# Kernel tuning notes

Measured on AMD Instinct MI355X. Metric: run time of the kernel, lower is better.

The kernel has to match this reference:

```python
import jax, jax.numpy as jnp
import numpy as np

N_E = 1024
E_DIM = 256
BETA = 0.25
PERSISTENCE = 0.1
B, T = 16, 1024


def setup_inputs() -> dict:
    key = jax.random.key(0)
    k1, k2 = jax.random.split(key)
    z = jax.random.normal(k1, (B, T, E_DIM), dtype=jnp.float32)
    # nn.Embedding(1+n_e, e_dim) init uniform(-1/n_e, 1/n_e)
    emb_weight = jax.random.uniform(k2, (N_E + 1, E_DIM), dtype=jnp.float32,
                                    minval=-1.0 / N_E, maxval=1.0 / N_E)
    return {"z": z, "emb_weight": emb_weight}


def _loss_contrast(z, ind, book):
    # z: (B,T,e), ind: (B,T) int, book: (n_e+1, e)
    z_q = book[ind]                                   # (B,T,e)
    loss_indices = jnp.sum((z - z_q) ** 2, axis=-1)   # (B,T)
    # ||z - book||^2 expanded to avoid the (B,T,n_e+1,e) intermediate
    z_sq = jnp.sum(z * z, axis=-1)                    # (B,T)
    b_sq = jnp.sum(book * book, axis=-1)              # (n_e+1,)
    cross = jnp.einsum('bte,ne->btn', z, book)        # (B,T,n_e+1)
    loss_all = z_sq[..., None] + b_sq[None, None, :] - 2.0 * cross
    lc = jnp.maximum(loss_indices[..., None] - loss_all + 1e-6 / N_E, 0.0)
    return jnp.mean(lc)


def _forward(z, emb_weight):
    zf = z.reshape(-1, E_DIM)
    d = (jnp.sum(zf * zf, axis=1, keepdims=True)
         + jnp.sum(emb_weight * emb_weight, axis=1)
         - 2.0 * (zf @ emb_weight.T)).reshape(B, T, N_E + 1)

    ind0 = jnp.clip(jnp.argmin(d[:, 0, :], axis=1), 0, N_E - 1)  # (B,)

    def step(carry, d_t):
        ind, coe = carry                              # (B,) int, (B,) f32
        d_here = jnp.take_along_axis(d_t, ind[:, None], axis=1)[:, 0]
        ind_next = jnp.minimum(ind + 1, N_E - 1)
        d_next = jnp.take_along_axis(d_t, ind_next[:, None], axis=1)[:, 0]
        stay = d_here <= d_next - coe
        ind_new = jnp.where(stay, ind, ind_next)
        coe_new = jnp.where(stay, coe + PERSISTENCE / N_E, 0.0)
        return (ind_new, coe_new), ind_new

    coe0 = jnp.zeros((B,), jnp.float32)
    _, inds = jax.lax.scan(step, (ind0, coe0), jnp.swapaxes(d[:, 1:, :], 0, 1))
    encoding_indices = jnp.concatenate([ind0[None, :], inds], axis=0).T  # (B,T)

    book_sg = jax.lax.stop_gradient(emb_weight)  # torch uses .data/.detach() everywhere
    z_q_raw = book_sg[encoding_indices]
    z_q = z + jax.lax.stop_gradient(z_q_raw - z)  # straight-through

    # non-legacy: beta * L(z, sg(book)) + L(sg(z), sg(book))
    loss = (BETA * _loss_contrast(z, encoding_indices, book_sg)
            + _loss_contrast(jax.lax.stop_gradient(z), encoding_indices, book_sg))

    v = jnp.max(encoding_indices) - jnp.min(encoding_indices)
    return z_q, loss, encoding_indices, v


def reference(z, emb_weight):
    return _forward(z, emb_weight)
```

## Files before the change

### kernel.cpp

```cpp
#include <hip/hip_runtime.h>

#define N_E   1024
#define EDIM  256
#define BB    16
#define TT    1024
#define NROW  (BB*TT)
#define NCOL  1025
#define NPAD  1152
#define PERS  (0.1f/1024.0f)
#define EPSC  (1e-6f/1024.0f)

#define OUT_LOSS 4194304
#define OUT_IDX  4194305
#define OUT_V    4210689

#define WS_ZB   0ull
#define WS_BBF  8388608ull
#define WS_BSQ  8978432ull
#define WS_E    8983552ull
#define WS_IND  84481024ull
#define WS_PART 84546560ull

typedef __attribute__((ext_vector_type(8))) short short8;
typedef __attribute__((ext_vector_type(4))) float floatx4;

__device__ __forceinline__ unsigned short f2bf(float f) {
    unsigned int u = __float_as_uint(f);
    u = (u + 0x7fffu + ((u >> 16) & 1u)) >> 16;
    return (unsigned short)u;
}

__device__ __forceinline__ float gload_f32(const float* p) {
    float r;
    asm volatile("global_load_dword %0, %1, off" : "=v"(r) : "v"(p));
    return r;
}

__global__ __launch_bounds__(256) void k0_prep(const float* __restrict__ z,
                                               const float* __restrict__ book,
                                               unsigned short* __restrict__ zb,
                                               unsigned short* __restrict__ bb,
                                               float* __restrict__ bsq) {
    int bx = blockIdx.x, tid = threadIdx.x;
    if (bx < 4096) {
        float4 v = ((const float4*)z)[bx * 256 + tid];
        size_t o = ((size_t)bx * 256 + tid) * 4;
        zb[o + 0] = f2bf(v.x); zb[o + 1] = f2bf(v.y);
        zb[o + 2] = f2bf(v.z); zb[o + 3] = f2bf(v.w);
    } else {
        int row = bx - 4096;
        float v = (row < NCOL) ? book[(size_t)row * EDIM + tid] : 0.0f;
        bb[(size_t)row * EDIM + tid] = f2bf(v);
        __shared__ float sd[256];
        sd[tid] = v * v;
        __syncthreads();
        for (int s = 128; s > 0; s >>= 1) { if (tid < s) sd[tid] += sd[tid + s]; __syncthreads(); }
        if (tid == 0) bsq[row] = sd[0];
    }
}

__global__ __launch_bounds__(256) void k1_gemm(const unsigned short* __restrict__ zb,
                                               const unsigned short* __restrict__ bb,
                                               const float* __restrict__ bsq,
                                               float* __restrict__ e) {
    int tid = threadIdx.x;
    int lane = tid & 63, w = tid >> 6;
    int mBase = blockIdx.x * 128 + (w >> 1) * 64;
    int nBase = blockIdx.y * 128 + (w & 1) * 64;
    int r = lane & 15, q = lane >> 4;

    floatx4 acc[4][4];
    #pragma unroll
    for (int i = 0; i < 4; i++)
        #pragma unroll
        for (int j = 0; j < 4; j++) acc[i][j] = (floatx4){0.f, 0.f, 0.f, 0.f};

    const short8* A = (const short8*)zb;
    const short8* Bm = (const short8*)bb;

    #pragma unroll
    for (int ks = 0; ks < 8; ks++) {
        int k8 = ks * 4 + q;
        short8 a[4], b[4];
        #pragma unroll
        for (int i = 0; i < 4; i++) a[i] = A[(size_t)(mBase + i * 16 + r) * 32 + k8];
        #pragma unroll
        for (int j = 0; j < 4; j++) b[j] = Bm[(size_t)(nBase + j * 16 + r) * 32 + k8];
        #pragma unroll
        for (int i = 0; i < 4; i++)
            #pragma unroll
            for (int j = 0; j < 4; j++)
                acc[i][j] = __builtin_amdgcn_mfma_f32_16x16x32_bf16(a[i], b[j], acc[i][j], 0, 0, 0);
    }

    float bsql[4];
    #pragma unroll
    for (int j = 0; j < 4; j++) bsql[j] = bsq[nBase + j * 16 + r];

    #pragma unroll
    for (int i = 0; i < 4; i++)
        #pragma unroll
        for (int rr = 0; rr < 4; rr++) {
            int m = mBase + i * 16 + q * 4 + rr;
            float* erow = e + (size_t)m * NPAD;
            #pragma unroll
            for (int j = 0; j < 4; j++)
                erow[nBase + j * 16 + r] = fmaf(-2.0f, acc[i][j][rr], bsql[j]);
        }
}


#define R15(X) X(0) X(1) X(2) X(3) X(4) X(5) X(6) X(7) X(8) X(9) X(10) X(11) X(12) X(13) X(14)

#define DECLA(i) float A0_##i, A1_##i, A2_##i; int q_##i;

#define LDR(S,i) { int _t = _tb + i; _t = _t < 1024 ? _t : 1023; \
                   A##S##_##i = gload_f32(_pe + (size_t)_t * NPAD); }
#define LD0(i) LDR(0,i)
#define LD1(i) LDR(1,i)
#define LD2(i) LDR(2,i)

#define QC(S,i) { float _bv = __shfl_down(A##S##_##i, 1, 64); \
                  int _qv = (int)((_bv - A##S##_##i) * QS); \
                  q_##i = _capn ? 0 : _qv; }
#define QC0(i) QC(0,i)
#define QC1(i) QC(1,i)
#define QC2(i) QC(2,i)

#define CH(i) { int _rel = ind - cb0; \
                int _qv = __builtin_amdgcn_readlane(q_##i, _rel); \
                bool _stay = (kk <= _qv); \
                int _ip1 = ind + 1; _ip1 = _ip1 < 1023 ? _ip1 : 1023; \
                ind = _stay ? ind : _ip1; \
                kk  = _stay ? kk + 1 : 0; \
                packed = (lane == i) ? ind : packed; }

#define ITER(SI, SC) { \
    int cbI = ind < 960 ? ind : 960; \
    { const float* _pe = eb + cbI + lane; int _tb = t + 45; R15(LD##SI) } \
    __builtin_amdgcn_sched_barrier(0); \
    int packed = 0; \
    R15(CH) \
    if (lane < 15 && t + lane < 1024) wind[ibase + t + lane] = packed; \
    __builtin_amdgcn_sched_barrier(0); \
    asm volatile("s_waitcnt vmcnt(31)" ::: "memory"); \
    __builtin_amdgcn_sched_barrier(0); \
    { bool _capn = (cb1 + lane == 1023); R15(QC##SC) } \
    cb0 = cb1; cb1 = cb2; cb2 = cbI; \
    t += 15; }

__global__ __launch_bounds__(256, 1) void k2_scan(const float* __restrict__ z,
                                                  const float* __restrict__ book,
                                                  const float* __restrict__ bsq,
                                                  const float* __restrict__ e,
                                                  int* __restrict__ wind) {
    __shared__ float sb[4]; __shared__ int si[4];

    int b = blockIdx.x, tid = threadIdx.x;
    int lane = tid & 63, w = tid >> 6;

    const float4* zr = (const float4*)(z + (size_t)b * TT * EDIM);
    float4 zv = zr[lane];
    float s = zv.x * zv.x + zv.y * zv.y + zv.z * zv.z + zv.w * zv.w;
    #pragma unroll
    for (int off = 32; off; off >>= 1) s += __shfl_xor(s, off, 64);
    float zsq = s;

    float best = 3.4e38f; int bidx = 0;
    for (int wi = w; wi < 17; wi += 4) {
        int n = wi * 64 + lane;
        if (n < NCOL) {
            const float4* br = (const float4*)(book + (size_t)n * EDIM);
            float c0 = 0.f, c1 = 0.f, c2 = 0.f, c3 = 0.f;
            #pragma unroll 8
            for (int k = 0; k < 64; k++) {
                float4 bo = br[k]; float4 za = zr[k];
                c0 = fmaf(za.x, bo.x, c0); c1 = fmaf(za.y, bo.y, c1);
                c2 = fmaf(za.z, bo.z, c2); c3 = fmaf(za.w, bo.w, c3);
            }
            float cr = (c0 + c1) + (c2 + c3);
            float d0 = (zsq + bsq[n]) - 2.0f * cr;
            if (d0 < best || (d0 == best && n < bidx)) { best = d0; bidx = n; }
        }
    }
    #pragma unroll
    for (int off = 32; off; off >>= 1) {
        float ob = __shfl_xor(best, off, 64);
        int   oi = __shfl_xor(bidx, off, 64);
        if (ob < best || (ob == best && oi < bidx)) { best = ob; bidx = oi; }
    }
    if (lane == 0) { sb[w] = best; si[w] = bidx; }
    __syncthreads();
    if (w != 0) return;

    best = sb[0]; bidx = si[0];
    for (int i = 1; i < 4; i++) {
        float vv = sb[i]; int ii = si[i];
        if (vv < best || (vv == best && ii < bidx)) { best = vv; bidx = ii; }
    }

    int ind = min(bidx, N_E - 1);
    int kk = 0;
    size_t ibase = (size_t)b * TT;
    if (lane == 0) wind[ibase] = ind;

    const float* eb = e + (size_t)b * TT * NPAD;
    const float QS = 1.0f / PERS;

    R15(DECLA)

    int cb0 = ind < 960 ? ind : 960;
    int cb1 = cb0, cb2 = cb0;
    { const float* _pe = eb + cb0 + lane; int _tb = 1;  R15(LD0) }
    { const float* _pe = eb + cb1 + lane; int _tb = 16; R15(LD1) }
    { const float* _pe = eb + cb2 + lane; int _tb = 31; R15(LD2) }
    asm volatile("s_waitcnt vmcnt(30)" ::: "memory");
    __builtin_amdgcn_sched_barrier(0);
    { bool _capn = (cb0 + lane == 1023); R15(QC0) }

    int t = 1;
    #pragma unroll 1
    for (int cc = 0; cc < 23; cc++) {
        ITER(0, 1)
        ITER(1, 2)
        ITER(2, 0)
    }
}

__global__ __launch_bounds__(256) void k3_loss_zq(const float* __restrict__ e,
                                                  const int* __restrict__ wind,
                                                  const float* __restrict__ book,
                                                  float* __restrict__ part,
                                                  float* __restrict__ out) {
    int rIdx = blockIdx.x, tid = threadIdx.x;
    int ind = wind[rIdx];
    const float* er = e + (size_t)rIdx * NPAD;
    float eind = er[ind];
    float p = 0.0f;
    for (int n = tid; n < NCOL; n += 256) {
        float v = eind - er[n] + EPSC;
        p += v > 0.0f ? v : 0.0f;
    }
    __shared__ float sd[256];
    sd[tid] = p; __syncthreads();
    for (int s = 128; s > 0; s >>= 1) { if (tid < s) sd[tid] += sd[tid + s]; __syncthreads(); }
    if (tid == 0) { part[rIdx] = sd[0]; out[OUT_IDX + rIdx] = (float)ind; }
    out[(size_t)rIdx * 256 + tid] = book[(size_t)ind * EDIM + tid];
}

__global__ __launch_bounds__(256) void k4_final(const float* __restrict__ part,
                                                const int* __restrict__ wind,
                                                float* __restrict__ out) {
    int tid = threadIdx.x;
    float s = 0.0f;
    for (int i = tid; i < NROW; i += 256) s += part[i];
    __shared__ float sd[256];
    sd[tid] = s; __syncthreads();
    for (int st = 128; st > 0; st >>= 1) { if (tid < st) sd[tid] += sd[tid + st]; __syncthreads(); }
    if (tid == 0) {
        int mn = wind[0], mx = wind[TT - 1];
        for (int b = 1; b < BB; b++) {
            mn = min(mn, wind[(size_t)b * TT]);
            mx = max(mx, wind[(size_t)b * TT + TT - 1]);
        }
        out[OUT_LOSS] = 1.25f * sd[0] / ((float)NROW * (float)NCOL);
        out[OUT_V] = (float)(mx - mn);
    }
}

extern "C" void kernel_launch(void* const* d_in, const int* in_sizes, int n_in,
                              void* d_out, int out_size, void* d_ws, size_t ws_size,
                              hipStream_t stream) {
    const float* z    = (const float*)d_in[0];
    const float* book = (const float*)d_in[1];
    char* ws = (char*)d_ws;
    unsigned short* zb = (unsigned short*)(ws + WS_ZB);
    unsigned short* bb = (unsigned short*)(ws + WS_BBF);
    float* bsq  = (float*)(ws + WS_BSQ);
    float* e    = (float*)(ws + WS_E);
    int*   wind = (int*)(ws + WS_IND);
    float* part = (float*)(ws + WS_PART);
    float* out  = (float*)d_out;

    hipLaunchKernelGGL(k0_prep,    dim3(4096 + 1152), dim3(256), 0, stream, z, book, zb, bb, bsq);
    hipLaunchKernelGGL(k1_gemm,    dim3(128, 9),      dim3(256), 0, stream, zb, bb, bsq, e);
    hipLaunchKernelGGL(k2_scan,    dim3(16),          dim3(256), 0, stream, z, book, bsq, e, wind);
    hipLaunchKernelGGL(k3_loss_zq, dim3(16384),       dim3(256), 0, stream, e, wind, book, part, out);
    hipLaunchKernelGGL(k4_final,   dim3(1),           dim3(256), 0, stream, part, wind, out);
}
```

Baseline: 251.4 us.

## Split scan window across half-waves and use double-buffered 10-step prefetch

```diff
diff --git a/kernel.cpp b/kernel.cpp
--- a/kernel.cpp
+++ b/kernel.cpp
@@ -110,44 +110,41 @@
 }
 
 
-#define R15(X) X(0) X(1) X(2) X(3) X(4) X(5) X(6) X(7) X(8) X(9) X(10) X(11) X(12) X(13) X(14)
-
-#define DECLA(i) float A0_##i, A1_##i, A2_##i; int q_##i;
-
-#define LDR(S,i) { int _t = _tb + i; _t = _t < 1024 ? _t : 1023; \
-                   A##S##_##i = gload_f32(_pe + (size_t)_t * NPAD); }
-#define LD0(i) LDR(0,i)
-#define LD1(i) LDR(1,i)
-#define LD2(i) LDR(2,i)
-
-#define QC(S,i) { float _bv = __shfl_down(A##S##_##i, 1, 64); \
-                  int _qv = (int)((_bv - A##S##_##i) * QS); \
-                  q_##i = _capn ? 0 : _qv; }
-#define QC0(i) QC(0,i)
-#define QC1(i) QC(1,i)
-#define QC2(i) QC(2,i)
-
-#define CH(i) { int _rel = ind - cb0; \
-                int _qv = __builtin_amdgcn_readlane(q_##i, _rel); \
-                bool _stay = (kk <= _qv); \
-                int _ip1 = ind + 1; _ip1 = _ip1 < 1023 ? _ip1 : 1023; \
-                ind = _stay ? ind : _ip1; \
-                kk  = _stay ? kk + 1 : 0; \
-                packed = (lane == i) ? ind : packed; }
-
-#define ITER(SI, SC) { \
-    int cbI = ind < 960 ? ind : 960; \
-    { const float* _pe = eb + cbI + lane; int _tb = t + 45; R15(LD##SI) } \
+#define DECLW float A0_0, A0_1, A0_2, A0_3, A0_4, A1_0, A1_1, A1_2, A1_3, A1_4; \
+              int q_0, q_1, q_2, q_3, q_4;
+
+#define LDOP(S,k) { int _t = _tb + 2*k + _g; _t = _t < 1024 ? _t : 1023; \
+                    A##S##_##k = gload_f32(_pe + (size_t)_t * NPAD); }
+#define LDSET(S) LDOP(S,0) LDOP(S,1) LDOP(S,2) LDOP(S,3) LDOP(S,4)
+
+#define QCOP(S,k) { float _bv = __shfl_down(A##S##_##k, 1, 32); \
+                    int _qv = (int)((_bv - A##S##_##k) * QS); \
+                    q_##k = _capn ? 0 : _qv; }
+#define QCSET(S) QCOP(S,0) QCOP(S,1) QCOP(S,2) QCOP(S,3) QCOP(S,4)
+
+#define CHS(j,k,h) { int _rel = ind - cbc; \
+                     int _qv = __builtin_amdgcn_readlane(q_##k, _rel + h); \
+                     bool _stay = (kk <= _qv); \
+                     int _ip1 = ind + 1; _ip1 = _ip1 < 1023 ? _ip1 : 1023; \
+                     ind = _stay ? ind : _ip1; \
+                     kk  = _stay ? kk + 1 : 0; \
+                     packed = (lane == j) ? ind : packed; }
+#define CHAIN CHS(0,0,0) CHS(1,0,32) CHS(2,1,0) CHS(3,1,32) CHS(4,2,0) \
+              CHS(5,2,32) CHS(6,3,0) CHS(7,3,32) CHS(8,4,0) CHS(9,4,32)
+
+#define ITERX(SI, SQ) { \
+    int cbI = ind < 992 ? ind : 992;                  \
+    { const float* _pe = eb + cbI + _cl; int _tb = t + 20; LDSET(SI) } \
     __builtin_amdgcn_sched_barrier(0); \
     int packed = 0; \
-    R15(CH) \
-    if (lane < 15 && t + lane < 1024) wind[ibase + t + lane] = packed; \
+    CHAIN \
+    if (lane < 10 && t + lane < 1024) wind[ibase + t + lane] = packed; \
     __builtin_amdgcn_sched_barrier(0); \
-    asm volatile("s_waitcnt vmcnt(31)" ::: "memory"); \
+    asm volatile("s_waitcnt vmcnt(6)" ::: "memory");  \
     __builtin_amdgcn_sched_barrier(0); \
-    { bool _capn = (cb1 + lane == 1023); R15(QC##SC) } \
-    cb0 = cb1; cb1 = cb2; cb2 = cbI; \
-    t += 15; }
+    { bool _capn = (cbn + _cl == 1023); QCSET(SQ) } \
+    cbc = cbn; cbn = cbI; \
+    t += 10; }
 
 __global__ __launch_bounds__(256, 1) void k2_scan(const float* __restrict__ z,
                                                   const float* __restrict__ book,
@@ -207,23 +204,24 @@
     const float* eb = e + (size_t)b * TT * NPAD;
     const float QS = 1.0f / PERS;
 
-    R15(DECLA)
-
-    int cb0 = ind < 960 ? ind : 960;
-    int cb1 = cb0, cb2 = cb0;
-    { const float* _pe = eb + cb0 + lane; int _tb = 1;  R15(LD0) }
-    { const float* _pe = eb + cb1 + lane; int _tb = 16; R15(LD1) }
-    { const float* _pe = eb + cb2 + lane; int _tb = 31; R15(LD2) }
-    asm volatile("s_waitcnt vmcnt(30)" ::: "memory");
+    int _g = lane >> 5;
+    int _cl = lane & 31;
+
+    DECLW
+
+    int cbc = ind < 992 ? ind : 992;
+    int cbn = cbc;
+    { const float* _pe = eb + cbc + _cl; int _tb = 1;  LDSET(0) }
+    { const float* _pe = eb + cbn + _cl; int _tb = 11; LDSET(1) }
+    asm volatile("s_waitcnt vmcnt(5)" ::: "memory");
     __builtin_amdgcn_sched_barrier(0);
-    { bool _capn = (cb0 + lane == 1023); R15(QC0) }
+    { bool _capn = (cbc + _cl == 1023); QCSET(0) }
 
     int t = 1;
     #pragma unroll 1
-    for (int cc = 0; cc < 23; cc++) {
-        ITER(0, 1)
-        ITER(1, 2)
-        ITER(2, 0)
+    for (int cc = 0; cc < 52; cc++) {
+        ITERX(0, 1)
+        ITERX(1, 0)
     }
 }
 
```

Result: faster. 241.0 us (-4.1%).
